# Kernel tuning notes

Hardware: AMD Instinct MI355X
Metric: run time of the kernel (lower is better)

The kernel has to match this reference:

```python
import jax, jax.numpy as jnp
import numpy as np

D_MODEL, D_STATE, D_CONV = 768, 8, 3
D_INNER = D_MODEL  # expand = 1
BATCH, SEQ = 4, 8192


def setup_inputs() -> dict:
    key = jax.random.key(0)
    ks = jax.random.split(key, 7)
    x = jax.random.normal(ks[0], (BATCH, SEQ, D_MODEL), dtype=jnp.float32)
    W_in = jax.random.normal(ks[1], (D_MODEL, 2 * D_INNER), dtype=jnp.float32) * 0.02
    conv_w = jax.random.normal(ks[2], (D_INNER, 1, D_CONV), dtype=jnp.float32) * 0.1
    conv_b = jnp.zeros((D_INNER,), dtype=jnp.float32)
    B = jax.random.normal(ks[3], (D_INNER, D_STATE), dtype=jnp.float32)
    C = jax.random.normal(ks[4], (D_INNER, D_STATE), dtype=jnp.float32)
    D = jnp.ones((D_INNER,), dtype=jnp.float32)
    W_out = jax.random.normal(ks[5], (D_INNER, D_MODEL), dtype=jnp.float32) * 0.02
    return {"x": x, "W_in": W_in, "conv_w": conv_w, "conv_b": conv_b,
            "B": B, "C": C, "D": D, "W_out": W_out}


def _forward(x, W_in, conv_w, conv_b, B, C, D, W_out):
    # in_proj and chunk
    xz = x @ W_in                                   # [B, L, 2*d_inner]
    xc, z = jnp.split(xz, 2, axis=-1)               # each [B, L, d_inner]
    # depthwise causal conv1d: torch pads (d_conv-1) both sides then slices [:L]
    # == left-pad (d_conv-1), no right pad
    xc = jnp.transpose(xc, (0, 2, 1))               # [B, d_inner, L]
    xc = jax.lax.conv_general_dilated(
        xc, conv_w,
        window_strides=(1,), padding=[(D_CONV - 1, 0)],
        dimension_numbers=("NCH", "OIH", "NCH"),
        feature_group_count=D_INNER)
    xc = xc + conv_b[None, :, None]
    xc = jnp.transpose(xc, (0, 2, 1))               # [B, L, d_inner]
    xc = jax.nn.silu(xc)
    z = jax.nn.silu(z)
    # simple SSM: h_t = h_{t-1} + outer(u_t, B); y_t = sum_s h_t*C + u_t*D
    # => y = cumsum_t(u) * sum_s(B*C) + u*D   (exact algebraic identity)
    BC = jnp.sum(B * C, axis=-1)                    # [d_inner]
    y = jnp.cumsum(xc, axis=1) * BC + xc * D
    out = (y * z) @ W_out                           # [B, L, d_model]
    return out


def reference(x, W_in, conv_w, conv_b, B, C, D, W_out):
    return _forward(x, W_in, conv_w, conv_b, B, C, D, W_out)
```

## Files before the change

kernel.cpp:

```cpp
#include <hip/hip_runtime.h>
#include <hip/hip_bf16.h>

#define D_MODEL 768
#define NSEQ    8192
#define NBATCH  4
#define MROWS   (NBATCH*NSEQ)
#define CHUNK   64
#define NCHUNK  (NSEQ/CHUNK)

#define BM 128
#define BN 128
#define BK 64

typedef __attribute__((ext_vector_type(8)))  short bshort8;
typedef __attribute__((ext_vector_type(16))) float f32x16;

__device__ __forceinline__ float bf2f(ushort u){
  union { unsigned int i; float f; } x; x.i = ((unsigned int)u) << 16; return x.f;
}
__device__ __forceinline__ ushort f2bf(float f){
  union { float f; unsigned int i; } x; x.f = f;
  unsigned int r = x.i + 0x7fffu + ((x.i >> 16) & 1u);
  return (ushort)(r >> 16);
}
__device__ __forceinline__ float silu_f(float v){ return v / (1.0f + __expf(-v)); }

__device__ __forceinline__ void async_copy16(const ushort* g, ushort* l){
  __builtin_amdgcn_global_load_lds((const __attribute__((address_space(1))) void*)g,
                                   (__attribute__((address_space(3))) void*)l, 16, 0, 0);
}

__global__ void tr_cvt(const float* __restrict__ in, ushort* __restrict__ out, int R, int C){
  __shared__ float tile[32][33];
  int c0 = blockIdx.x*32, r0 = blockIdx.y*32;
  int tx = threadIdx.x & 31, ty = threadIdx.x >> 5;
  #pragma unroll
  for (int p=0;p<4;p++){
    int r = ty + p*8;
    tile[r][tx] = in[(size_t)(r0+r)*C + c0 + tx];
  }
  __syncthreads();
  #pragma unroll
  for (int p=0;p<4;p++){
    int c = ty + p*8;
    out[(size_t)(c0+c)*R + r0 + tx] = f2bf(tile[tx][c]);
  }
}

__global__ void cvt_bf16(const float* __restrict__ in, ushort* __restrict__ out, int n){
  int i = (blockIdx.x*256 + threadIdx.x)*8;
  if (i >= n) return;
  const float4 f0 = *(const float4*)(in + i);
  const float4 f1 = *(const float4*)(in + i + 4);
  ushort o[8];
  o[0]=f2bf(f0.x); o[1]=f2bf(f0.y); o[2]=f2bf(f0.z); o[3]=f2bf(f0.w);
  o[4]=f2bf(f1.x); o[5]=f2bf(f1.y); o[6]=f2bf(f1.z); o[7]=f2bf(f1.w);
  *(ulonglong2*)(out + i) = *(const ulonglong2*)o;
}

__global__ __launch_bounds__(256,3) void gemm1_bt(
    const ushort* __restrict__ A, const ushort* __restrict__ BT,
    ushort* __restrict__ oxc, ushort* __restrict__ oz, int K)
{
  __shared__ __align__(16) ushort Asm[BM*BK];
  __shared__ __align__(16) ushort Bsm[BN*BK];
  const int tid = threadIdx.x;
  const int bm = blockIdx.x, bn = blockIdx.y;
  const int lane = tid & 63, wid = tid >> 6;
  const int wm = (wid >> 1) * 64, wn = (wid & 1) * 64;
  const int l31 = lane & 31, half = lane >> 5;

  const ushort* Ag[4]; ushort* Al[4];
  #pragma unroll
  for (int it=0; it<4; ++it){
    int p  = it*256 + tid;
    int r  = p >> 3;
    int cl = (p & 7) ^ (r & 7);
    Ag[it] = A + (size_t)(bm*BM + r)*K + cl*8;
    Al[it] = Asm + p*8;
  }
  const ushort* Bg[4]; ushort* Bl[4];
  #pragma unroll
  for (int it=0; it<4; ++it){
    int p  = it*256 + tid;
    int r  = p >> 3;
    int cl = (p & 7) ^ (r & 7);
    Bg[it] = BT + (size_t)(bn*BN + r)*K + cl*8;
    Bl[it] = Bsm + p*8;
  }

  int arow[2], ar7[2], brow[2], br7[2];
  #pragma unroll
  for (int i=0;i<2;i++){
    int ra = wm + i*32 + l31; arow[i] = ra*BK; ar7[i] = ra & 7;
  }
  #pragma unroll
  for (int j=0;j<2;j++){
    int rb = wn + j*32 + l31; brow[j] = rb*BK; br7[j] = rb & 7;
  }

  f32x16 acc[2][2];
  #pragma unroll
  for (int i=0;i<2;i++)
    #pragma unroll
    for (int j=0;j<2;j++)
      #pragma unroll
      for (int r=0;r<16;r++) acc[i][j][r] = 0.f;

  const int KT = K / BK;
  for (int kt=0; kt<KT; ++kt){
    __syncthreads();
    #pragma unroll
    for (int it=0; it<4; ++it){ async_copy16(Ag[it], Al[it]); Ag[it] += BK; }
    #pragma unroll
    for (int it=0; it<4; ++it){ async_copy16(Bg[it], Bl[it]); Bg[it] += BK; }
    asm volatile("s_waitcnt vmcnt(0)" ::: "memory");
    __syncthreads();

    #pragma unroll
    for (int s=0; s<4; ++s){
      const int c = s*2 + half;
      bshort8 av[2], bv[2];
      #pragma unroll
      for (int i=0;i<2;i++)
        av[i] = *(const bshort8*)(Asm + arow[i] + ((c ^ ar7[i]) << 3));
      #pragma unroll
      for (int j=0;j<2;j++)
        bv[j] = *(const bshort8*)(Bsm + brow[j] + ((c ^ br7[j]) << 3));
      #pragma unroll
      for (int i=0;i<2;i++)
        #pragma unroll
        for (int j=0;j<2;j++)
          acc[i][j] = __builtin_amdgcn_mfma_f32_32x32x16_bf16(av[i], bv[j], acc[i][j], 0,0,0);
    }
  }

  if (bn < 6){
    #pragma unroll
    for (int i=0;i<2;i++){
      const int Rbase = bm*BM + wm + i*32 + 4*half;
      #pragma unroll
      for (int j=0;j<2;j++){
        const int Cc = bn*BN + wn + j*32 + l31;
        #pragma unroll
        for (int reg=0; reg<16; reg++){
          const int R = Rbase + (reg & 3) + 8*(reg >> 2);
          oxc[(size_t)R*768 + Cc] = f2bf(acc[i][j][reg]);
        }
      }
    }
  } else {
    #pragma unroll
    for (int i=0;i<2;i++){
      const int Rbase = bm*BM + wm + i*32 + 4*half;
      #pragma unroll
      for (int j=0;j<2;j++){
        const int Cc = bn*BN - 768 + wn + j*32 + l31;
        #pragma unroll
        for (int reg=0; reg<16; reg++){
          const int R = Rbase + (reg & 3) + 8*(reg >> 2);
          oz[(size_t)R*768 + Cc] = f2bf(silu_f(acc[i][j][reg]));
        }
      }
    }
  }
}

__global__ __launch_bounds__(256,3) void gemm2_bt(
    const ushort* __restrict__ A, const ushort* __restrict__ BT,
    float* __restrict__ of, int K)
{
  __shared__ __align__(16) ushort Asm[BM*BK];
  __shared__ __align__(16) ushort Bsm[BN*BK];
  const int tid = threadIdx.x;
  const int bm = blockIdx.x, bn = blockIdx.y;
  const int lane = tid & 63, wid = tid >> 6;
  const int wm = (wid >> 1) * 64, wn = (wid & 1) * 64;
  const int l31 = lane & 31, half = lane >> 5;

  const ushort* Ag[4]; ushort* Al[4];
  #pragma unroll
  for (int it=0; it<4; ++it){
    int p  = it*256 + tid;
    int r  = p >> 3;
    int cl = (p & 7) ^ (r & 7);
    Ag[it] = A + (size_t)(bm*BM + r)*K + cl*8;
    Al[it] = Asm + p*8;
  }
  const ushort* Bg[4]; ushort* Bl[4];
  #pragma unroll
  for (int it=0; it<4; ++it){
    int p  = it*256 + tid;
    int r  = p >> 3;
    int cl = (p & 7) ^ (r & 7);
    Bg[it] = BT + (size_t)(bn*BN + r)*K + cl*8;
    Bl[it] = Bsm + p*8;
  }

  int arow[2], ar7[2], brow[2], br7[2];
  #pragma unroll
  for (int i=0;i<2;i++){
    int ra = wm + i*32 + l31; arow[i] = ra*BK; ar7[i] = ra & 7;
  }
  #pragma unroll
  for (int j=0;j<2;j++){
    int rb = wn + j*32 + l31; brow[j] = rb*BK; br7[j] = rb & 7;
  }

  f32x16 acc[2][2];
  #pragma unroll
  for (int i=0;i<2;i++)
    #pragma unroll
    for (int j=0;j<2;j++)
      #pragma unroll
      for (int r=0;r<16;r++) acc[i][j][r] = 0.f;

  const int KT = K / BK;
  for (int kt=0; kt<KT; ++kt){
    __syncthreads();
    #pragma unroll
    for (int it=0; it<4; ++it){ async_copy16(Ag[it], Al[it]); Ag[it] += BK; }
    #pragma unroll
    for (int it=0; it<4; ++it){ async_copy16(Bg[it], Bl[it]); Bg[it] += BK; }
    asm volatile("s_waitcnt vmcnt(0)" ::: "memory");
    __syncthreads();

    #pragma unroll
    for (int s=0; s<4; ++s){
      const int c = s*2 + half;
      bshort8 av[2], bv[2];
      #pragma unroll
      for (int i=0;i<2;i++)
        av[i] = *(const bshort8*)(Asm + arow[i] + ((c ^ ar7[i]) << 3));
      #pragma unroll
      for (int j=0;j<2;j++)
        bv[j] = *(const bshort8*)(Bsm + brow[j] + ((c ^ br7[j]) << 3));
      #pragma unroll
      for (int i=0;i<2;i++)
        #pragma unroll
        for (int j=0;j<2;j++)
          acc[i][j] = __builtin_amdgcn_mfma_f32_32x32x16_bf16(av[i], bv[j], acc[i][j], 0,0,0);
    }
  }

  #pragma unroll
  for (int i=0;i<2;i++){
    const int Rbase = bm*BM + wm + i*32 + 4*half;
    #pragma unroll
    for (int j=0;j<2;j++){
      const int Cc = bn*BN + wn + j*32 + l31;
      #pragma unroll
      for (int reg=0; reg<16; reg++){
        const int R = Rbase + (reg & 3) + 8*(reg >> 2);
        of[(size_t)R*768 + Cc] = acc[i][j][reg];
      }
    }
  }
}

__global__ void conv_psum(const ushort* __restrict__ xc, const float* __restrict__ cw,
                          const float* __restrict__ cb, float* __restrict__ psum){
  int c = threadIdx.x;
  int b = blockIdx.z, ch = blockIdx.x;
  int t0 = ch*CHUNK;
  const ushort* xp = xc + (size_t)b*NSEQ*768 + c;
  float w0=cw[c*3+0], w1=cw[c*3+1], w2=cw[c*3+2], bia=cb[c];
  float m2=0.f, m1=0.f;
  if (t0>=2) m2 = bf2f(xp[(size_t)(t0-2)*768]);
  if (t0>=1) m1 = bf2f(xp[(size_t)(t0-1)*768]);
  float s=0.f;
  #pragma unroll 4
  for (int i=0;i<CHUNK;i++){
    float x = bf2f(xp[(size_t)(t0+i)*768]);
    s += silu_f(w0*m2 + w1*m1 + w2*x + bia);
    m2=m1; m1=x;
  }
  psum[((size_t)b*NCHUNK + ch)*768 + c] = s;
}

__global__ void scan_chunks(const float* __restrict__ psum, float* __restrict__ offs){
  int idx = blockIdx.x*256 + threadIdx.x;
  int b = idx/768, c = idx%768;
  float run = 0.f;
  #pragma unroll 8
  for (int ch=0; ch<NCHUNK; ch++){
    size_t o = ((size_t)b*NCHUNK + ch)*768 + c;
    offs[o] = run;
    run += psum[o];
  }
}

__global__ void scan_apply(const ushort* __restrict__ xc, const ushort* __restrict__ zb,
                           const float* __restrict__ cw, const float* __restrict__ cb,
                           const float* __restrict__ Bm, const float* __restrict__ Cm,
                           const float* __restrict__ Dv, const float* __restrict__ offs,
                           ushort* __restrict__ v){
  int c = threadIdx.x;
  int b = blockIdx.z, ch = blockIdx.x;
  int t0 = ch*CHUNK;
  size_t base = (size_t)b*NSEQ*768 + c;
  const ushort* xp = xc + base;
  const ushort* zp = zb + base;
  ushort* vp = v + base;
  float w0=cw[c*3+0], w1=cw[c*3+1], w2=cw[c*3+2], bia=cb[c];
  float bc=0.f;
  #pragma unroll
  for (int s=0;s<8;s++) bc += Bm[c*8+s]*Cm[c*8+s];
  float dd = Dv[c];
  float cu = offs[((size_t)b*NCHUNK + ch)*768 + c];
  float m2=0.f, m1=0.f;
  if (t0>=2) m2 = bf2f(xp[(size_t)(t0-2)*768]);
  if (t0>=1) m1 = bf2f(xp[(size_t)(t0-1)*768]);
  #pragma unroll 4
  for (int i=0;i<CHUNK;i++){
    size_t o = (size_t)(t0+i)*768;
    float x = bf2f(xp[o]);
    float z = bf2f(zp[o]);
    float u = silu_f(w0*m2 + w1*m1 + w2*x + bia);
    cu += u;
    float y = bc*cu + dd*u;
    vp[o] = f2bf(y * z);
    m2=m1; m1=x;
  }
}

extern "C" void kernel_launch(void* const* d_in, const int* in_sizes, int n_in,
                              void* d_out, int out_size, void* d_ws, size_t ws_size,
                              hipStream_t stream)
{
  const float* x      = (const float*)d_in[0];
  const float* W_in   = (const float*)d_in[1];
  const float* conv_w = (const float*)d_in[2];
  const float* conv_b = (const float*)d_in[3];
  const float* Bm     = (const float*)d_in[4];
  const float* Cm     = (const float*)d_in[5];
  const float* Dv     = (const float*)d_in[6];
  const float* W_out  = (const float*)d_in[7];
  float* out = (float*)d_out;

  char* ws = (char*)d_ws;
  ushort* xbf   = (ushort*)(ws + 0);
  ushort* xcbf  = (ushort*)(ws + 50331648);
  ushort* zbf   = (ushort*)(ws + 100663296);
  ushort* wint  = (ushort*)(ws + 150994944);
  ushort* woutt = (ushort*)(ws + 153354240);
  float*  psum  = (float*)(ws + 154533888);
  float*  offs  = (float*)(ws + 150994944);
  if (ws_size < 156106752) return;

  tr_cvt<<<dim3(1536/32, 768/32), 256, 0, stream>>>(W_in,  wint,  768, 1536);
  tr_cvt<<<dim3(768/32,  768/32), 256, 0, stream>>>(W_out, woutt, 768, 768);
  cvt_bf16<<<(MROWS*768)/2048, 256, 0, stream>>>(x, xbf, MROWS*768);

  gemm1_bt<<<dim3(MROWS/BM, 1536/BN), 256, 0, stream>>>(xbf, wint, xcbf, zbf, 768);

  conv_psum  <<<dim3(NCHUNK, 1, NBATCH), 768, 0, stream>>>(xcbf, conv_w, conv_b, psum);
  scan_chunks<<<12, 256, 0, stream>>>(psum, offs);
  scan_apply <<<dim3(NCHUNK, 1, NBATCH), 768, 0, stream>>>(xcbf, zbf, conv_w, conv_b,
                                                           Bm, Cm, Dv, offs, xbf );

  gemm2_bt<<<dim3(MROWS/BM, 768/BN), 256, 0, stream>>>(xbf, woutt, out, 768);
}
```

Measured before the change: 390.9 us.

## Replace GEMMs with 256x256 double-buffered 8-wave pipelined MFMA kernel

Both projection GEMMs now use a single templated kernel with 256x256 output tiles, 8 waves and 16x16x32 MFMAs instead of 128x128 tiles with 32x32 MFMAs. K tiles are double-buffered in LDS with async global-to-LDS copies interleaved between MFMA phases, synchronised by explicit barriers, waitcnts and setprio. The goal is to overlap memory loads with compute and raise data reuse per tile. In exchange the kernel uses more LDS and registers, which limits occupancy, and the wave grid is small relative to the CU count.

```diff
diff --git a/kernel.cpp b/kernel.cpp
--- a/kernel.cpp
+++ b/kernel.cpp
@@ -8,12 +8,8 @@
 #define CHUNK   64
 #define NCHUNK  (NSEQ/CHUNK)
 
-#define BM 128
-#define BN 128
-#define BK 64
-
 typedef __attribute__((ext_vector_type(8)))  short bshort8;
-typedef __attribute__((ext_vector_type(16))) float f32x16;
+typedef __attribute__((ext_vector_type(4)))  float f32x4;
 
 __device__ __forceinline__ float bf2f(ushort u){
   union { unsigned int i; float f; } x; x.i = ((unsigned int)u) << 16; return x.f;
@@ -58,204 +54,151 @@
   *(ulonglong2*)(out + i) = *(const ulonglong2*)o;
 }
 
-__global__ __launch_bounds__(256,3) void gemm1_bt(
+
+__device__ __forceinline__ void ldsA_f(const ushort* AHd, int mhofs, int rbase,
+                                       const int cof0, const int cof1, bshort8 a[4][2]){
+  #pragma unroll
+  for (int fm=0; fm<4; ++fm){
+    a[fm][0] = *(const bshort8*)(AHd + mhofs + fm*1024 + rbase + cof0);
+    a[fm][1] = *(const bshort8*)(AHd + mhofs + fm*1024 + rbase + cof1);
+  }
+}
+__device__ __forceinline__ void ldsB_f(const ushort* BP0, const ushort* BP1, int rbase,
+                                       const int cof0, const int cof1, bshort8 b[2][2]){
+  b[0][0] = *(const bshort8*)(BP0 + rbase + cof0);
+  b[0][1] = *(const bshort8*)(BP0 + rbase + cof1);
+  b[1][0] = *(const bshort8*)(BP1 + rbase + cof0);
+  b[1][1] = *(const bshort8*)(BP1 + rbase + cof1);
+}
+__device__ __forceinline__ void mmq_f(const bshort8 a[4][2], const bshort8 b[2][2],
+                                      f32x4 (*accq)[4], int nb){
+  #pragma unroll
+  for (int fm=0; fm<4; ++fm){
+    #pragma unroll
+    for (int fn=0; fn<2; ++fn){
+      accq[fm][nb+fn] = __builtin_amdgcn_mfma_f32_16x16x32_bf16(a[fm][0], b[fn][0], accq[fm][nb+fn], 0,0,0);
+      accq[fm][nb+fn] = __builtin_amdgcn_mfma_f32_16x16x32_bf16(a[fm][1], b[fn][1], accq[fm][nb+fn], 0,0,0);
+    }
+  }
+}
+
+#define PH_SYNC  do{ __builtin_amdgcn_sched_barrier(0); __builtin_amdgcn_s_barrier(); \
+  asm volatile("s_waitcnt lgkmcnt(0)" ::: "memory"); __builtin_amdgcn_sched_barrier(0); \
+  __builtin_amdgcn_s_setprio(1); }while(0)
+#define PH_END   do{ __builtin_amdgcn_s_setprio(0); __builtin_amdgcn_sched_barrier(0); \
+  __builtin_amdgcn_s_barrier(); }while(0)
+#define PH_ENDV  do{ __builtin_amdgcn_s_setprio(0); __builtin_amdgcn_sched_barrier(0); \
+  asm volatile("s_waitcnt vmcnt(2)" ::: "memory"); __builtin_amdgcn_s_barrier(); }while(0)
+
+template<int MODE>
+__global__ __launch_bounds__(512,2) void gemm8(
     const ushort* __restrict__ A, const ushort* __restrict__ BT,
-    ushort* __restrict__ oxc, ushort* __restrict__ oz, int K)
+    ushort* __restrict__ oxc, ushort* __restrict__ oz,
+    float* __restrict__ of, int K)
 {
-  __shared__ __align__(16) ushort Asm[BM*BK];
-  __shared__ __align__(16) ushort Bsm[BN*BK];
-  const int tid = threadIdx.x;
-  const int bm = blockIdx.x, bn = blockIdx.y;
+  __shared__ __align__(16) ushort L[2][2][2][128*64];
+  const int tid  = threadIdx.x;
+  const int bm   = blockIdx.x, bn = blockIdx.y;
   const int lane = tid & 63, wid = tid >> 6;
-  const int wm = (wid >> 1) * 64, wn = (wid & 1) * 64;
-  const int l31 = lane & 31, half = lane >> 5;
-
-  const ushort* Ag[4]; ushort* Al[4];
-  #pragma unroll
-  for (int it=0; it<4; ++it){
-    int p  = it*256 + tid;
-    int r  = p >> 3;
-    int cl = (p & 7) ^ (r & 7);
-    Ag[it] = A + (size_t)(bm*BM + r)*K + cl*8;
-    Al[it] = Asm + p*8;
-  }
-  const ushort* Bg[4]; ushort* Bl[4];
-  #pragma unroll
-  for (int it=0; it<4; ++it){
-    int p  = it*256 + tid;
-    int r  = p >> 3;
-    int cl = (p & 7) ^ (r & 7);
-    Bg[it] = BT + (size_t)(bn*BN + r)*K + cl*8;
-    Bl[it] = Bsm + p*8;
-  }
-
-  int arow[2], ar7[2], brow[2], br7[2];
-  #pragma unroll
-  for (int i=0;i<2;i++){
-    int ra = wm + i*32 + l31; arow[i] = ra*BK; ar7[i] = ra & 7;
-  }
-  #pragma unroll
-  for (int j=0;j<2;j++){
-    int rb = wn + j*32 + l31; brow[j] = rb*BK; br7[j] = rb & 7;
-  }
-
-  f32x16 acc[2][2];
-  #pragma unroll
-  for (int i=0;i<2;i++)
+  const int wm   = wid >> 2;
+  const int wn   = wid & 3;
+  const int l15  = lane & 15, lh = lane >> 4;
+
+  const int p0i = tid, p1i = 512 + tid;
+  const int r0s = p0i >> 3, c0s = (p0i & 7) ^ (r0s & 7);
+  const int r1s = p1i >> 3, c1s = (p1i & 7) ^ (r1s & 7);
+  const int ro0 = r0s*K + c0s*8, ro1 = r1s*K + c1s*8;
+  const int so0 = p0i*8,         so1 = p1i*8;
+
+  const ushort* Agb[2] = { A  + (size_t)(bm*256)*K, A  + (size_t)(bm*256 + 128)*K };
+  const ushort* Bgb[2] = { BT + (size_t)(bn*256)*K, BT + (size_t)(bn*256 + 128)*K };
+
+#define STGH(mat,h,t,d) do{ const ushort* _g = ((mat)? Bgb[h] : Agb[h]) + (t)*64; \
+  ushort* _l = &L[d][mat][h][0]; \
+  async_copy16(_g + ro0, _l + so0); async_copy16(_g + ro1, _l + so1); }while(0)
+
+  const int cof0 = ((0*4 + lh) ^ (l15 & 7)) * 8;
+  const int cof1 = ((1*4 + lh) ^ (l15 & 7)) * 8;
+  const int rbase = l15 * 64;
+  const ushort* AH[2] = { &L[0][0][wm][0], &L[1][0][wm][0] };
+  const ushort* BP[2][2][2];
+  #pragma unroll
+  for (int d=0; d<2; ++d)
     #pragma unroll
-    for (int j=0;j<2;j++)
+    for (int nh=0; nh<2; ++nh)
       #pragma unroll
-      for (int r=0;r<16;r++) acc[i][j][r] = 0.f;
-
-  const int KT = K / BK;
-  for (int kt=0; kt<KT; ++kt){
-    __syncthreads();
+      for (int fn=0; fn<2; ++fn){
+        int off_n = wn*64 + nh*32 + fn*16;
+        BP[d][nh][fn] = &L[d][1][off_n>>7][(off_n & 127)*64];
+      }
+
+  f32x4 acc[8][4];
+  #pragma unroll
+  for (int m=0;m<8;m++)
     #pragma unroll
-    for (int it=0; it<4; ++it){ async_copy16(Ag[it], Al[it]); Ag[it] += BK; }
+    for (int n=0;n<4;n++)
+      #pragma unroll
+      for (int r=0;r<4;r++) acc[m][n][r] = 0.f;
+
+  bshort8 a[4][2], b0[2][2], b1[2][2];
+
+  STGH(0,0,0,0); STGH(0,1,0,0); STGH(1,0,0,0); STGH(1,1,0,0);
+  STGH(0,0,1,1); STGH(0,1,1,1); STGH(1,0,1,1); STGH(1,1,1,1);
+  __builtin_amdgcn_sched_barrier(0);
+  asm volatile("s_waitcnt vmcnt(8)" ::: "memory");
+  __builtin_amdgcn_s_barrier();
+
+  for (int i=0; i<6; ++i){
+    const int t1 = 2*i + 1;
+    const int t2 = (i<5) ? 2*i + 2 : 0;
+    const int t3 = (i<5) ? 2*i + 3 : 1;
+    ldsA_f(AH[0], 0,    rbase, cof0, cof1, a);
+    ldsB_f(BP[0][0][0], BP[0][0][1], rbase, cof0, cof1, b0);
+    STGH(0,1,t1,1);
+    PH_SYNC; mmq_f(a, b0, &acc[0], 0); PH_END;
+    ldsB_f(BP[0][1][0], BP[0][1][1], rbase, cof0, cof1, b1);
+    STGH(1,0,t1,1);
+    PH_SYNC; mmq_f(a, b1, &acc[0], 2); PH_END;
+    ldsA_f(AH[0], 64*64, rbase, cof0, cof1, a);
+    STGH(1,1,t1,1);
+    PH_SYNC; mmq_f(a, b0, &acc[4], 0); PH_END;
+    STGH(0,0,t2,0);
+    PH_SYNC; mmq_f(a, b1, &acc[4], 2); PH_ENDV;
+    ldsA_f(AH[1], 0,    rbase, cof0, cof1, a);
+    ldsB_f(BP[1][0][0], BP[1][0][1], rbase, cof0, cof1, b0);
+    STGH(0,1,t2,0);
+    PH_SYNC; mmq_f(a, b0, &acc[0], 0); PH_END;
+    ldsB_f(BP[1][1][0], BP[1][1][1], rbase, cof0, cof1, b1);
+    STGH(1,0,t2,0);
+    PH_SYNC; mmq_f(a, b1, &acc[0], 2); PH_END;
+    ldsA_f(AH[1], 64*64, rbase, cof0, cof1, a);
+    STGH(1,1,t2,0);
+    PH_SYNC; mmq_f(a, b0, &acc[4], 0); PH_END;
+    STGH(0,0,t3,1);
+    PH_SYNC; mmq_f(a, b1, &acc[4], 2); PH_ENDV;
+  }
+  asm volatile("s_waitcnt vmcnt(0)" ::: "memory");
+
+  #pragma unroll
+  for (int m=0;m<8;m++){
+    const int Rb = bm*256 + wm*128 + m*16 + lh*4;
     #pragma unroll
-    for (int it=0; it<4; ++it){ async_copy16(Bg[it], Bl[it]); Bg[it] += BK; }
-    asm volatile("s_waitcnt vmcnt(0)" ::: "memory");
-    __syncthreads();
-
-    #pragma unroll
-    for (int s=0; s<4; ++s){
-      const int c = s*2 + half;
-      bshort8 av[2], bv[2];
+    for (int n=0;n<4;n++){
+      const int Cc = bn*256 + wn*64 + n*16 + l15;
       #pragma unroll
-      for (int i=0;i<2;i++)
-        av[i] = *(const bshort8*)(Asm + arow[i] + ((c ^ ar7[i]) << 3));
-      #pragma unroll
-      for (int j=0;j<2;j++)
-        bv[j] = *(const bshort8*)(Bsm + brow[j] + ((c ^ br7[j]) << 3));
-      #pragma unroll
-      for (int i=0;i<2;i++)
-        #pragma unroll
-        for (int j=0;j<2;j++)
-          acc[i][j] = __builtin_amdgcn_mfma_f32_32x32x16_bf16(av[i], bv[j], acc[i][j], 0,0,0);
-    }
-  }
-
-  if (bn < 6){
-    #pragma unroll
-    for (int i=0;i<2;i++){
-      const int Rbase = bm*BM + wm + i*32 + 4*half;
-      #pragma unroll
-      for (int j=0;j<2;j++){
-        const int Cc = bn*BN + wn + j*32 + l31;
-        #pragma unroll
-        for (int reg=0; reg<16; reg++){
-          const int R = Rbase + (reg & 3) + 8*(reg >> 2);
-          oxc[(size_t)R*768 + Cc] = f2bf(acc[i][j][reg]);
+      for (int r=0;r<4;r++){
+        const float v = acc[m][n][r];
+        const int R = Rb + r;
+        if constexpr (MODE==1){
+          if (bn < 3) oxc[(size_t)R*768 + Cc] = f2bf(v);
+          else        oz [(size_t)R*768 + (Cc-768)] = f2bf(silu_f(v));
+        } else {
+          of[(size_t)R*768 + Cc] = v;
         }
       }
     }
-  } else {
-    #pragma unroll
-    for (int i=0;i<2;i++){
-      const int Rbase = bm*BM + wm + i*32 + 4*half;
-      #pragma unroll
-      for (int j=0;j<2;j++){
-        const int Cc = bn*BN - 768 + wn + j*32 + l31;
-        #pragma unroll
-        for (int reg=0; reg<16; reg++){
-          const int R = Rbase + (reg & 3) + 8*(reg >> 2);
-          oz[(size_t)R*768 + Cc] = f2bf(silu_f(acc[i][j][reg]));
-        }
-      }
-    }
-  }
-}
-
-__global__ __launch_bounds__(256,3) void gemm2_bt(
-    const ushort* __restrict__ A, const ushort* __restrict__ BT,
-    float* __restrict__ of, int K)
-{
-  __shared__ __align__(16) ushort Asm[BM*BK];
-  __shared__ __align__(16) ushort Bsm[BN*BK];
-  const int tid = threadIdx.x;
-  const int bm = blockIdx.x, bn = blockIdx.y;
-  const int lane = tid & 63, wid = tid >> 6;
-  const int wm = (wid >> 1) * 64, wn = (wid & 1) * 64;
-  const int l31 = lane & 31, half = lane >> 5;
-
-  const ushort* Ag[4]; ushort* Al[4];
-  #pragma unroll
-  for (int it=0; it<4; ++it){
-    int p  = it*256 + tid;
-    int r  = p >> 3;
-    int cl = (p & 7) ^ (r & 7);
-    Ag[it] = A + (size_t)(bm*BM + r)*K + cl*8;
-    Al[it] = Asm + p*8;
-  }
-  const ushort* Bg[4]; ushort* Bl[4];
-  #pragma unroll
-  for (int it=0; it<4; ++it){
-    int p  = it*256 + tid;
-    int r  = p >> 3;
-    int cl = (p & 7) ^ (r & 7);
-    Bg[it] = BT + (size_t)(bn*BN + r)*K + cl*8;
-    Bl[it] = Bsm + p*8;
-  }
-
-  int arow[2], ar7[2], brow[2], br7[2];
-  #pragma unroll
-  for (int i=0;i<2;i++){
-    int ra = wm + i*32 + l31; arow[i] = ra*BK; ar7[i] = ra & 7;
-  }
-  #pragma unroll
-  for (int j=0;j<2;j++){
-    int rb = wn + j*32 + l31; brow[j] = rb*BK; br7[j] = rb & 7;
-  }
-
-  f32x16 acc[2][2];
-  #pragma unroll
-  for (int i=0;i<2;i++)
-    #pragma unroll
-    for (int j=0;j<2;j++)
-      #pragma unroll
-      for (int r=0;r<16;r++) acc[i][j][r] = 0.f;
-
-  const int KT = K / BK;
-  for (int kt=0; kt<KT; ++kt){
-    __syncthreads();
-    #pragma unroll
-    for (int it=0; it<4; ++it){ async_copy16(Ag[it], Al[it]); Ag[it] += BK; }
-    #pragma unroll
-    for (int it=0; it<4; ++it){ async_copy16(Bg[it], Bl[it]); Bg[it] += BK; }
-    asm volatile("s_waitcnt vmcnt(0)" ::: "memory");
-    __syncthreads();
-
-    #pragma unroll
-    for (int s=0; s<4; ++s){
-      const int c = s*2 + half;
-      bshort8 av[2], bv[2];
-      #pragma unroll
-      for (int i=0;i<2;i++)
-        av[i] = *(const bshort8*)(Asm + arow[i] + ((c ^ ar7[i]) << 3));
-      #pragma unroll
-      for (int j=0;j<2;j++)
-        bv[j] = *(const bshort8*)(Bsm + brow[j] + ((c ^ br7[j]) << 3));
-      #pragma unroll
-      for (int i=0;i<2;i++)
-        #pragma unroll
-        for (int j=0;j<2;j++)
-          acc[i][j] = __builtin_amdgcn_mfma_f32_32x32x16_bf16(av[i], bv[j], acc[i][j], 0,0,0);
-    }
-  }
-
-  #pragma unroll
-  for (int i=0;i<2;i++){
-    const int Rbase = bm*BM + wm + i*32 + 4*half;
-    #pragma unroll
-    for (int j=0;j<2;j++){
-      const int Cc = bn*BN + wn + j*32 + l31;
-      #pragma unroll
-      for (int reg=0; reg<16; reg++){
-        const int R = Rbase + (reg & 3) + 8*(reg >> 2);
-        of[(size_t)R*768 + Cc] = acc[i][j][reg];
-      }
-    }
-  }
+  }
+#undef STGH
 }
 
 __global__ void conv_psum(const ushort* __restrict__ xc, const float* __restrict__ cw,
@@ -352,12 +295,12 @@
   tr_cvt<<<dim3(768/32,  768/32), 256, 0, stream>>>(W_out, woutt, 768, 768);
   cvt_bf16<<<(MROWS*768)/2048, 256, 0, stream>>>(x, xbf, MROWS*768);
 
-  gemm1_bt<<<dim3(MROWS/BM, 1536/BN), 256, 0, stream>>>(xbf, wint, xcbf, zbf, 768);
+  gemm8<1><<<dim3(MROWS/256, 1536/256), 512, 0, stream>>>(xbf, wint, xcbf, zbf, nullptr, 768);
 
   conv_psum  <<<dim3(NCHUNK, 1, NBATCH), 768, 0, stream>>>(xcbf, conv_w, conv_b, psum);
   scan_chunks<<<12, 256, 0, stream>>>(psum, offs);
   scan_apply <<<dim3(NCHUNK, 1, NBATCH), 768, 0, stream>>>(xcbf, zbf, conv_w, conv_b,
                                                            Bm, Cm, Dv, offs, xbf );
 
-  gemm2_bt<<<dim3(MROWS/BM, 768/BN), 256, 0, stream>>>(xbf, woutt, out, 768);
-}
+  gemm8<2><<<dim3(MROWS/256, 768/256), 512, 0, stream>>>(xbf, woutt, nullptr, nullptr, out, 768);
+}
```

After: 385.8 us. About the same (-1.3%).
